# Performance work log

Measured on AMD Instinct MI355X. Metric: run time of the kernel, lower is better.

## Reference

```python
import jax, jax.numpy as jnp
import numpy as np

EPS = 1e-5

def _conv1x1(x, w, b):
    # x: (b,c,t,h,w), w: (o,c), b: (o,)  -> (b,o,t,h,w)
    return jnp.einsum('bcthw,oc->bothw', x, w) + b[None, :, None, None, None]

def setup_inputs() -> dict:
    key = jax.random.key(0)
    ks = jax.random.split(key, 12)
    B, C, IC, T, H, W = 32, 1024, 512, 8, 16, 8
    s_c = 1.0 / np.sqrt(C)
    s_ic = 1.0 / np.sqrt(IC)
    return {
        'x':       jax.random.normal(ks[0], (B, C, T, H, W), jnp.float32),
        'g_w':     jax.random.normal(ks[1], (IC, C), jnp.float32) * s_c,
        'g_b':     jax.random.normal(ks[2], (IC,), jnp.float32) * 0.01,
        'theta_w': jax.random.normal(ks[3], (IC, C), jnp.float32) * s_c,
        'theta_b': jax.random.normal(ks[4], (IC,), jnp.float32) * 0.01,
        'phi_w':   jax.random.normal(ks[5], (IC, C), jnp.float32) * s_c,
        'phi_b':   jax.random.normal(ks[6], (IC,), jnp.float32) * 0.01,
        'w_w':     jax.random.normal(ks[7], (C, IC), jnp.float32) * s_ic,
        'w_b':     jax.random.normal(ks[8], (C,), jnp.float32) * 0.01,
        'bn_gamma': jax.random.normal(ks[9], (C,), jnp.float32) * 0.1 + 1.0,
        'bn_beta':  jax.random.normal(ks[10], (C,), jnp.float32) * 0.01,
        'bn_mean':  jax.random.normal(ks[11], (C,), jnp.float32) * 0.01,
        'bn_var':   jnp.ones((C,), jnp.float32),
    }

def reference(x, g_w, g_b, theta_w, theta_b, phi_w, phi_b, w_w, w_b,
              bn_gamma, bn_beta, bn_mean, bn_var):
    B, C, T, H, W = x.shape
    IC = g_w.shape[0]
    # value projection, flattened per frame: (b, t, ic*h*w)
    g_x = _conv1x1(x, g_w, g_b)                       # (b,ic,t,h,w)
    g_x = jnp.transpose(g_x, (0, 2, 1, 3, 4)).reshape(B, T, IC * H * W)
    # pooled query/key over spatial dims: (b,t,ic) and (b,ic,t)
    theta = _conv1x1(x, theta_w, theta_b).mean(axis=(3, 4))   # (b,ic,t)
    phi = _conv1x1(x, phi_w, phi_b).mean(axis=(3, 4))         # (b,ic,t)
    f = jnp.einsum('bct,bcs->bts', theta, phi)                # (b,t,t)
    attn = jax.nn.softmax(f, axis=-1)
    y = jnp.einsum('bts,bsd->btd', attn, g_x)                 # (b,t,ic*h*w)
    y = jnp.transpose(y.reshape(B, T, IC, H, W), (0, 2, 1, 3, 4))  # (b,ic,t,h,w)
    # output projection + BatchNorm3d (inference stats) + residual
    wy = _conv1x1(y, w_w, w_b)                        # (b,c,t,h,w)
    inv = bn_gamma / jnp.sqrt(bn_var + EPS)
    wy = wy * inv[None, :, None, None, None] + (bn_beta - bn_mean * inv)[None, :, None, None, None]
    return wy + x
```

## Files before the change

### kernel.cpp

```cpp
#include <hip/hip_runtime.h>
#include <hip/hip_bf16.h>

typedef __attribute__((ext_vector_type(8))) short bf16x8;
typedef __attribute__((ext_vector_type(4))) float f32x4;

#if defined(__has_builtin)
#if __has_builtin(__builtin_amdgcn_global_load_lds)
#define USE_GLOAD_LDS 1
#endif
#endif

__device__ __forceinline__ void gload_lds16(const void* g, void* ldsbase) {
#ifdef USE_GLOAD_LDS
    __builtin_amdgcn_global_load_lds(
        (__attribute__((address_space(1))) void*)(g),
        (__attribute__((address_space(3))) void*)(ldsbase), 16, 0, 0);
#endif
}

__global__ __launch_bounds__(256) void early_kernel(
        const float* __restrict__ x, float* __restrict__ xbar,
        const float* __restrict__ gw, const float* __restrict__ ww,
        __hip_bfloat16* __restrict__ gwt, __hip_bfloat16* __restrict__ wwb,
        const float* __restrict__ gb, const float* __restrict__ wb,
        const float* __restrict__ gamma, const float* __restrict__ beta,
        const float* __restrict__ mean, const float* __restrict__ var,
        float* __restrict__ inv, float* __restrict__ shift) {
    __shared__ float tile[32][33];
    int bid = blockIdx.x;
    int tid = threadIdx.x;
    if (bid < 16384) {
        int row = bid * 16 + (tid >> 4);
        int j = tid & 15;
        const float4* p = (const float4*)(x + (size_t)row * 128);
        float4 a = p[j * 2], b2 = p[j * 2 + 1];
        float s = a.x + a.y + a.z + a.w + b2.x + b2.y + b2.z + b2.w;
        s += __shfl_xor(s, 1); s += __shfl_xor(s, 2);
        s += __shfl_xor(s, 4); s += __shfl_xor(s, 8);
        if (j == 0) xbar[row] = s * (1.0f / 128.0f);
    } else if (bid < 16896) {
        int b2 = bid - 16384;
        int icb = b2 >> 5, cb = b2 & 31;
        int r = tid >> 5, c = tid & 31;
        #pragma unroll
        for (int i = 0; i < 4; i++)
            tile[r + i * 8][c] = gw[(size_t)(icb * 32 + r + i * 8) * 1024 + cb * 32 + c];
        __syncthreads();
        #pragma unroll
        for (int i = 0; i < 4; i++) {
            int cin = cb * 32 + r + i * 8;
            gwt[(size_t)cin * 512 + icb * 32 + c] = __float2bfloat16(tile[c][r + i * 8]);
        }
    } else if (bid < 17152) {
        int b2 = bid - 16896;
        size_t base = (size_t)b2 * 2048 + (size_t)tid * 8;
        const float4* src = (const float4*)(ww + base);
        float4 v0 = src[0], v1 = src[1];
        __hip_bfloat16 tmp[8];
        tmp[0] = __float2bfloat16(v0.x); tmp[1] = __float2bfloat16(v0.y);
        tmp[2] = __float2bfloat16(v0.z); tmp[3] = __float2bfloat16(v0.w);
        tmp[4] = __float2bfloat16(v1.x); tmp[5] = __float2bfloat16(v1.y);
        tmp[6] = __float2bfloat16(v1.z); tmp[7] = __float2bfloat16(v1.w);
        *(bf16x8*)(wwb + base) = *(const bf16x8*)tmp;
    } else {
        int b2 = bid - 17152;
        int wv = tid >> 6, l = tid & 63;
        int c = b2 * 32 + wv * 8 + (l >> 3);
        int j = l & 7;
        const float* wr = ww + (size_t)c * 512;
        float acc = 0.0f;
        #pragma unroll 8
        for (int k = j; k < 512; k += 8) acc += wr[k] * gb[k];
        acc += __shfl_xor(acc, 1); acc += __shfl_xor(acc, 2); acc += __shfl_xor(acc, 4);
        if (j == 0) {
            float cb2 = wb[c] + acc;
            float iv = gamma[c] * rsqrtf(var[c] + 1e-5f);
            inv[c] = iv;
            shift[c] = cb2 * iv + beta[c] - mean[c] * iv;
        }
    }
}

__global__ __launch_bounds__(256) void stage2_kernel(
        const float* __restrict__ xbar,
        const float* __restrict__ tw, const float* __restrict__ tb,
        const float* __restrict__ pw, const float* __restrict__ pb,
        float* __restrict__ theta, float* __restrict__ phi,
        const __hip_bfloat16* __restrict__ wwb,
        const __hip_bfloat16* __restrict__ gwt,
        __hip_bfloat16* __restrict__ M) {
    __shared__ __align__(16) char smem[32768];
    int bid = blockIdx.x;
    int tid = threadIdx.x;
    if (bid < 1024) {
        float* xs = (float*)smem;
        int which = bid & 1;
        int icc = (bid >> 1) & 15;
        int b = bid >> 5;
        const float* w = which ? pw : tw;
        const float* bias = which ? pb : tb;
        float* out = which ? phi : theta;
        for (int i = tid; i < 8192; i += 256) xs[i] = xbar[b * 8192 + i];
        __syncthreads();
        int icl = tid >> 3;
        int t = tid & 7;
        int ic = icc * 32 + icl;
        const float* wr = w + (size_t)ic * 1024;
        float acc = 0.0f;
        #pragma unroll 8
        for (int k = 0; k < 1024; k++) acc += wr[k] * xs[k * 8 + t];
        out[((size_t)b * 512 + ic) * 8 + t] = acc + bias[ic];
    } else {
        __hip_bfloat16* As = (__hip_bfloat16*)smem;
        __hip_bfloat16* Bs = (__hip_bfloat16*)(smem + 8192);
        int b2 = bid - 1024;
        int mb = b2 >> 3, nb = b2 & 7;
        int c0 = mb * 128, n0 = nb * 128;
        int w = tid >> 6, l = tid & 63;
        int wr = w >> 1, wc = w & 1;
        const __hip_bfloat16* Ab = wwb + (size_t)c0 * 512;
        const __hip_bfloat16* Bb = gwt + (size_t)n0 * 512;
        int arow = tid >> 2, akq = tid & 3;
        f32x4 acc[4][4] = {};
        for (int kk = 0; kk < 16; ++kk) {
            int k0 = kk * 32;
#ifdef USE_GLOAD_LDS
            gload_lds16(Ab + (size_t)arow * 512 + k0 + akq * 8,        (char*)As + w * 1024);
            gload_lds16(Ab + (size_t)(arow + 64) * 512 + k0 + akq * 8, (char*)As + 4096 + w * 1024);
            gload_lds16(Bb + (size_t)arow * 512 + k0 + akq * 8,        (char*)Bs + w * 1024);
            gload_lds16(Bb + (size_t)(arow + 64) * 512 + k0 + akq * 8, (char*)Bs + 4096 + w * 1024);
#else
            *(bf16x8*)((char*)As + (size_t)tid * 16)        = *(const bf16x8*)(Ab + (size_t)arow * 512 + k0 + akq * 8);
            *(bf16x8*)((char*)As + 4096 + (size_t)tid * 16) = *(const bf16x8*)(Ab + (size_t)(arow + 64) * 512 + k0 + akq * 8);
            *(bf16x8*)((char*)Bs + (size_t)tid * 16)        = *(const bf16x8*)(Bb + (size_t)arow * 512 + k0 + akq * 8);
            *(bf16x8*)((char*)Bs + 4096 + (size_t)tid * 16) = *(const bf16x8*)(Bb + (size_t)(arow + 64) * 512 + k0 + akq * 8);
#endif
            __syncthreads();
            const __hip_bfloat16* Ap = As + ((size_t)(wr * 64 + (l & 15)) * 32) + (l >> 4) * 8;
            const __hip_bfloat16* Bp = Bs + ((size_t)(wc * 64 + (l & 15)) * 32) + (l >> 4) * 8;
            bf16x8 af[4], bfr[4];
            #pragma unroll
            for (int m = 0; m < 4; m++) af[m] = *(const bf16x8*)(Ap + m * 16 * 32);
            #pragma unroll
            for (int n = 0; n < 4; n++) bfr[n] = *(const bf16x8*)(Bp + n * 16 * 32);
            #pragma unroll
            for (int m = 0; m < 4; m++)
                #pragma unroll
                for (int n = 0; n < 4; n++)
                    acc[m][n] = __builtin_amdgcn_mfma_f32_16x16x32_bf16(af[m], bfr[n], acc[m][n], 0, 0, 0);
            __syncthreads();
        }
        int col = l & 15, rg = l >> 4;
        #pragma unroll
        for (int m = 0; m < 4; m++)
            #pragma unroll
            for (int j = 0; j < 4; j++) {
                int gc = c0 + wr * 64 + m * 16 + rg * 4 + j;
                #pragma unroll
                for (int n = 0; n < 4; n++)
                    M[(size_t)gc * 1024 + n0 + wc * 64 + n * 16 + col] = __float2bfloat16(acc[m][n][j]);
            }
    }
}

__global__ __launch_bounds__(64) void attn_kernel(const float* __restrict__ theta,
                                                  const float* __restrict__ phi,
                                                  float* __restrict__ attn) {
    __shared__ float th[4096], ph[4096];
    int b = blockIdx.x, lane = threadIdx.x;
    for (int i = lane; i < 4096; i += 64) {
        th[i] = theta[(size_t)b * 4096 + i];
        ph[i] = phi[(size_t)b * 4096 + i];
    }
    __syncthreads();
    int t = lane >> 3, s = lane & 7;
    float f = 0.0f;
    #pragma unroll 8
    for (int ic = 0; ic < 512; ic++) f += th[ic * 8 + t] * ph[ic * 8 + s];
    float m = f;
    m = fmaxf(m, __shfl_xor(m, 1));
    m = fmaxf(m, __shfl_xor(m, 2));
    m = fmaxf(m, __shfl_xor(m, 4));
    float e = __expf(f - m);
    float sum = e;
    sum += __shfl_xor(sum, 1); sum += __shfl_xor(sum, 2); sum += __shfl_xor(sum, 4);
    attn[b * 64 + lane] = e / sum;
}

__global__ __launch_bounds__(256) void mix_kernel(const float* __restrict__ x,
                                                  const float* __restrict__ attn,
                                                  __hip_bfloat16* __restrict__ xmt) {
    int orig = blockIdx.x;
    int wg = (orig & 7) * 64 + (orig >> 3);
    int b = wg >> 4;
    int hwg = wg & 15;
    __shared__ float at[64];
    __shared__ float xs[8][8][33];
    int tid = threadIdx.x;
    if (tid < 64) at[tid] = attn[b * 64 + tid];
    int ci = tid >> 3, s = tid & 7;
    int h = tid >> 5, cq = tid & 31;
    const float* xb = x + ((size_t)b << 20);
    __hip_bfloat16* ob = xmt + ((size_t)b << 20);
    for (int cc = 0; cc < 32; ++cc) {
        const float4* src = (const float4*)(xb + ((size_t)(cc * 32 + ci) * 8 + s) * 128 + hwg * 8);
        float4 v0 = src[0], v1 = src[1];
        __syncthreads();
        xs[s][0][ci] = v0.x; xs[s][1][ci] = v0.y; xs[s][2][ci] = v0.z; xs[s][3][ci] = v0.w;
        xs[s][4][ci] = v1.x; xs[s][5][ci] = v1.y; xs[s][6][ci] = v1.z; xs[s][7][ci] = v1.w;
        __syncthreads();
        float xr[8];
        #pragma unroll
        for (int ss = 0; ss < 8; ss++) xr[ss] = xs[ss][h][cq];
        #pragma unroll
        for (int t = 0; t < 8; t++) {
            float o = 0.0f;
            #pragma unroll
            for (int ss = 0; ss < 8; ss++) o += at[t * 8 + ss] * xr[ss];
            ob[(size_t)(t * 128 + hwg * 8 + h) * 1024 + cc * 32 + cq] = __float2bfloat16(o);
        }
    }
}

__global__ __launch_bounds__(256, 3) void gemm128_kernel(
        const __hip_bfloat16* __restrict__ Mw,
        const __hip_bfloat16* __restrict__ xmt,
        const float* __restrict__ x,
        const float* __restrict__ inv, const float* __restrict__ shift,
        float* __restrict__ out) {
    __shared__ __align__(16) __hip_bfloat16 HBs[16384];
    char* AH = (char*)HBs;
    const int BUFB = 16384;

    int orig = blockIdx.x;
    int bid = (orig & 7) * 256 + (orig >> 3);
    int b = bid >> 6;
    int mb = (bid >> 3) & 7;
    int nb = bid & 7;
    int c0 = mb * 128, n0 = nb * 128;

    int tid = threadIdx.x;
    int w = tid >> 6, l = tid & 63;
    int wr = w >> 1, wc = w & 1;

    int sgl = (((l & 3) - ((l >> 3) & 3)) & 3);
    const __hip_bfloat16* aS = Mw + (size_t)(c0 + w * 16 + (l >> 2)) * 1024 + sgl * 8;
    const __hip_bfloat16* bS = xmt + ((size_t)b << 20) + (size_t)(n0 + w * 16 + (l >> 2)) * 1024 + sgl * 8;
    int stBase = w * 1024;

    int rdSlot = ((l >> 4) + (((l & 15) >> 1) & 3)) & 3;
    int aRdBase = (wr * 64 + (l & 15)) * 64 + rdSlot * 16;
    int bRdBase = 8192 + (wc * 64 + (l & 15)) * 64 + rdSlot * 16;

    f32x4 acc[4][4] = {};

    #define ISSUE(q) do {                                                       \
        gload_lds16(aS,             AH + (q) * BUFB + stBase);                  \
        gload_lds16(aS + 64 * 1024, AH + (q) * BUFB + 4096 + stBase);           \
        gload_lds16(bS,             AH + (q) * BUFB + 8192 + stBase);           \
        gload_lds16(bS + 64 * 1024, AH + (q) * BUFB + 12288 + stBase);          \
        aS += 32; bS += 32;                                                     \
    } while (0)

    #define V4 asm volatile("s_waitcnt vmcnt(4)" ::: "memory")
    #define V0 asm volatile("s_waitcnt vmcnt(0)" ::: "memory")
    #define SB0 __builtin_amdgcn_sched_barrier(0)
    #define BAR __builtin_amdgcn_s_barrier()
    #define LGKM0 asm volatile("s_waitcnt lgkmcnt(0)" ::: "memory")

    #define HSTEP(q, MODE) do {                                                 \
        const char* bp = AH + (q) * BUFB;                                       \
        bf16x8 af0 = *(const bf16x8*)(bp + aRdBase);                            \
        bf16x8 af1 = *(const bf16x8*)(bp + aRdBase + 1024);                     \
        bf16x8 af2 = *(const bf16x8*)(bp + aRdBase + 2048);                     \
        bf16x8 af3 = *(const bf16x8*)(bp + aRdBase + 3072);                     \
        bf16x8 bf0 = *(const bf16x8*)(bp + bRdBase);                            \
        bf16x8 bf1 = *(const bf16x8*)(bp + bRdBase + 1024);                     \
        bf16x8 bf2 = *(const bf16x8*)(bp + bRdBase + 2048);                     \
        bf16x8 bf3 = *(const bf16x8*)(bp + bRdBase + 3072);                     \
        LGKM0; SB0;                                                             \
        BAR;                                  \
        if ((MODE) == 0) ISSUE(q);              \
        SB0;                                                                    \
        __builtin_amdgcn_s_setprio(1);                                          \
        _Pragma("unroll")                                                       \
        for (int n = 0; n < 4; ++n) {                                           \
            bf16x8 bfn = (n == 0) ? bf0 : (n == 1) ? bf1 : (n == 2) ? bf2 : bf3;\
            acc[0][n] = __builtin_amdgcn_mfma_f32_16x16x32_bf16(af0, bfn, acc[0][n], 0, 0, 0); \
            acc[1][n] = __builtin_amdgcn_mfma_f32_16x16x32_bf16(af1, bfn, acc[1][n], 0, 0, 0); \
            acc[2][n] = __builtin_amdgcn_mfma_f32_16x16x32_bf16(af2, bfn, acc[2][n], 0, 0, 0); \
            acc[3][n] = __builtin_amdgcn_mfma_f32_16x16x32_bf16(af3, bfn, acc[3][n], 0, 0, 0); \
        }                                                                       \
        __builtin_amdgcn_s_setprio(0);                                          \
        SB0;                                                                    \
        if ((MODE) == 0) { V4; BAR; SB0; }                                      \
        else if ((MODE) == 1) { V0; BAR; SB0; }                                 \
    } while (0)

    ISSUE(0); ISSUE(1);
    V4; BAR; SB0;

    #pragma unroll 1
    for (int t = 0; t < 15; ++t) {
        HSTEP(0, 0);
        HSTEP(1, 0);
    }
    HSTEP(0, 1);
    HSTEP(1, 2);

    #undef ISSUE
    #undef HSTEP
    #undef V4
    #undef V0
    #undef SB0
    #undef BAR
    #undef LGKM0

    int col = l & 15, rg = l >> 4;
    const float* xb = x + ((size_t)b << 20);
    float* ob = out + ((size_t)b << 20);
    #pragma unroll
    for (int mi = 0; mi < 4; ++mi) {
        #pragma unroll
        for (int j = 0; j < 4; ++j) {
            int gc = c0 + wr * 64 + mi * 16 + rg * 4 + j;
            float iv = inv[gc], sh = shift[gc];
            size_t rowoff = (size_t)gc * 1024 + n0 + wc * 64 + col;
            #pragma unroll
            for (int n = 0; n < 4; ++n) {
                size_t idx = rowoff + n * 16;
                ob[idx] = acc[mi][n][j] * iv + sh + xb[idx];
            }
        }
    }
}

extern "C" void kernel_launch(void* const* d_in, const int* in_sizes, int n_in,
                              void* d_out, int out_size, void* d_ws, size_t ws_size,
                              hipStream_t stream) {
    const float* x    = (const float*)d_in[0];
    const float* g_w  = (const float*)d_in[1];
    const float* g_b  = (const float*)d_in[2];
    const float* th_w = (const float*)d_in[3];
    const float* th_b = (const float*)d_in[4];
    const float* ph_w = (const float*)d_in[5];
    const float* ph_b = (const float*)d_in[6];
    const float* w_w  = (const float*)d_in[7];
    const float* w_b  = (const float*)d_in[8];
    const float* gam  = (const float*)d_in[9];
    const float* bet  = (const float*)d_in[10];
    const float* mea  = (const float*)d_in[11];
    const float* var  = (const float*)d_in[12];
    float* out = (float*)d_out;
    char* ws = (char*)d_ws;

    __hip_bfloat16* xmt = (__hip_bfloat16*)ws;
    __hip_bfloat16* Mw  = (__hip_bfloat16*)(ws + 67108864);
    float* xbar  = (float*)(ws + 69206016);
    float* theta = (float*)(ws + 70254592);
    float* phi   = (float*)(ws + 70778880);
    float* attn  = (float*)(ws + 71303168);
    float* inv   = (float*)(ws + 71311360);
    float* shift = (float*)(ws + 71315456);
    __hip_bfloat16* gwt = (__hip_bfloat16*)ws;
    __hip_bfloat16* wwb = (__hip_bfloat16*)(ws + 1048576);

    hipLaunchKernelGGL(early_kernel, dim3(17184), dim3(256), 0, stream,
                       x, xbar, g_w, w_w, gwt, wwb,
                       g_b, w_b, gam, bet, mea, var, inv, shift);
    hipLaunchKernelGGL(stage2_kernel, dim3(1088), dim3(256), 0, stream,
                       xbar, th_w, th_b, ph_w, ph_b, theta, phi, wwb, gwt, Mw);
    hipLaunchKernelGGL(attn_kernel, dim3(32), dim3(64), 0, stream, theta, phi, attn);
    hipLaunchKernelGGL(mix_kernel, dim3(512), dim3(256), 0, stream, x, attn, xmt);
    hipLaunchKernelGGL(gemm128_kernel, dim3(2048), dim3(256), 0, stream,
                       Mw, xmt, x, inv, shift, out);
}
```

Baseline: 233.5 us.

## Restructure mix kernel tiling and vectorize theta/phi projection loads

The mix kernel now assigns each block a 32-channel slab of one batch. It loads the whole slab contiguously with float4 reads, converts it to bf16 in LDS, and applies the temporal attention mixing for all spatial positions, using twice as many blocks. The theta/phi projection in stage2 transposes xbar into a padded t-major LDS layout so that both weights and activations can be read as float4 with two accumulators. The aim is coalesced global reads and fewer barriers, at the cost of more LDS per block in mix, which may limit occupancy. Rounding x to bf16 before mixing, rather than after, slightly changes numerics.

Measured after the change: 219.6 us. 1.06x faster.

```diff
diff --git a/kernel.cpp b/kernel.cpp
--- a/kernel.cpp
+++ b/kernel.cpp
@@ -16,6 +16,11 @@
         (__attribute__((address_space(1))) void*)(g),
         (__attribute__((address_space(3))) void*)(ldsbase), 16, 0, 0);
 #endif
+}
+
+__device__ __forceinline__ unsigned short f2bf(float f) {
+    __hip_bfloat16 h = __float2bfloat16(f);
+    return *reinterpret_cast<unsigned short*>(&h);
 }
 
 __global__ __launch_bounds__(256) void early_kernel(
@@ -89,7 +94,7 @@
         const __hip_bfloat16* __restrict__ wwb,
         const __hip_bfloat16* __restrict__ gwt,
         __hip_bfloat16* __restrict__ M) {
-    __shared__ __align__(16) char smem[32768];
+    __shared__ __align__(16) char smem[33024];
     int bid = blockIdx.x;
     int tid = threadIdx.x;
     if (bid < 1024) {
@@ -100,16 +105,36 @@
         const float* w = which ? pw : tw;
         const float* bias = which ? pb : tb;
         float* out = which ? phi : theta;
-        for (int i = tid; i < 8192; i += 256) xs[i] = xbar[b * 8192 + i];
+        const float* xbb = xbar + b * 8192;
+        #pragma unroll
+        for (int k = 0; k < 8; ++k) {
+            int f4 = tid + k * 256;
+            float4 v = *(const float4*)(xbb + (size_t)f4 * 4);
+            int c = f4 >> 1;
+            int t0 = (f4 & 1) * 4;
+            xs[(t0 + 0) * 1028 + c] = v.x;
+            xs[(t0 + 1) * 1028 + c] = v.y;
+            xs[(t0 + 2) * 1028 + c] = v.z;
+            xs[(t0 + 3) * 1028 + c] = v.w;
+        }
         __syncthreads();
-        int icl = tid >> 3;
-        int t = tid & 7;
+        int icl = tid >> 3, t = tid & 7;
         int ic = icc * 32 + icl;
         const float* wr = w + (size_t)ic * 1024;
-        float acc = 0.0f;
-        #pragma unroll 8
-        for (int k = 0; k < 1024; k++) acc += wr[k] * xs[k * 8 + t];
-        out[((size_t)b * 512 + ic) * 8 + t] = acc + bias[ic];
+        const float* xr = xs + t * 1028;
+        float a0 = 0.0f, a1 = 0.0f;
+        #pragma unroll 4
+        for (int k = 0; k < 1024; k += 8) {
+            float4 wv0 = *(const float4*)(wr + k);
+            float4 wv1 = *(const float4*)(wr + k + 4);
+            float4 xv0 = *(const float4*)(xr + k);
+            float4 xv1 = *(const float4*)(xr + k + 4);
+            a0 = fmaf(wv0.x, xv0.x, a0); a0 = fmaf(wv0.y, xv0.y, a0);
+            a0 = fmaf(wv0.z, xv0.z, a0); a0 = fmaf(wv0.w, xv0.w, a0);
+            a1 = fmaf(wv1.x, xv1.x, a1); a1 = fmaf(wv1.y, xv1.y, a1);
+            a1 = fmaf(wv1.z, xv1.z, a1); a1 = fmaf(wv1.w, xv1.w, a1);
+        }
+        out[((size_t)b * 512 + ic) * 8 + t] = a0 + a1 + bias[ic];
     } else {
         __hip_bfloat16* As = (__hip_bfloat16*)smem;
         __hip_bfloat16* Bs = (__hip_bfloat16*)(smem + 8192);
@@ -191,33 +216,49 @@
                                                   const float* __restrict__ attn,
                                                   __hip_bfloat16* __restrict__ xmt) {
     int orig = blockIdx.x;
-    int wg = (orig & 7) * 64 + (orig >> 3);
-    int b = wg >> 4;
-    int hwg = wg & 15;
+    int wg = (orig & 7) * 128 + (orig >> 3);
+    int b = wg >> 5;
+    int c0 = (wg & 31) * 32;
     __shared__ float at[64];
-    __shared__ float xs[8][8][33];
+    __shared__ __align__(8) unsigned short xls[32 * 1028];
     int tid = threadIdx.x;
     if (tid < 64) at[tid] = attn[b * 64 + tid];
-    int ci = tid >> 3, s = tid & 7;
-    int h = tid >> 5, cq = tid & 31;
-    const float* xb = x + ((size_t)b << 20);
-    __hip_bfloat16* ob = xmt + ((size_t)b << 20);
-    for (int cc = 0; cc < 32; ++cc) {
-        const float4* src = (const float4*)(xb + ((size_t)(cc * 32 + ci) * 8 + s) * 128 + hwg * 8);
-        float4 v0 = src[0], v1 = src[1];
-        __syncthreads();
-        xs[s][0][ci] = v0.x; xs[s][1][ci] = v0.y; xs[s][2][ci] = v0.z; xs[s][3][ci] = v0.w;
-        xs[s][4][ci] = v1.x; xs[s][5][ci] = v1.y; xs[s][6][ci] = v1.z; xs[s][7][ci] = v1.w;
-        __syncthreads();
-        float xr[8];
-        #pragma unroll
-        for (int ss = 0; ss < 8; ss++) xr[ss] = xs[ss][h][cq];
-        #pragma unroll
-        for (int t = 0; t < 8; t++) {
-            float o = 0.0f;
-            #pragma unroll
-            for (int ss = 0; ss < 8; ss++) o += at[t * 8 + ss] * xr[ss];
-            ob[(size_t)(t * 128 + hwg * 8 + h) * 1024 + cc * 32 + cq] = __float2bfloat16(o);
+    const float* xb = x + ((size_t)b << 20) + (size_t)c0 * 1024;
+    #pragma unroll
+    for (int k = 0; k < 32; ++k) {
+        int f4 = tid + k * 256;
+        float4 v = *(const float4*)(xb + (size_t)f4 * 4);
+        int ci = f4 >> 8;
+        int rem = (f4 & 255) * 4;
+        unsigned short h[4];
+        h[0] = f2bf(v.x); h[1] = f2bf(v.y); h[2] = f2bf(v.z); h[3] = f2bf(v.w);
+        *(ushort4*)(&xls[ci * 1028 + rem]) = *(const ushort4*)h;
+    }
+    __syncthreads();
+    int ci = tid & 31, h2 = tid >> 5;
+    const unsigned short* basep = &xls[ci * 1028];
+    __hip_bfloat16* ob = xmt + ((size_t)b << 20) + c0 + ci;
+    #pragma unroll
+    for (int i = 0; i < 8; ++i) {
+        int hw0 = (h2 + 8 * i) * 2;
+        float o0[8] = {}, o1[8] = {};
+        #pragma unroll
+        for (int s = 0; s < 8; ++s) {
+            unsigned int pr = *(const unsigned int*)(basep + s * 128 + hw0);
+            float v0 = __uint_as_float(pr << 16);
+            float v1 = __uint_as_float(pr & 0xffff0000u);
+            #pragma unroll
+            for (int t = 0; t < 8; ++t) {
+                float a = at[t * 8 + s];
+                o0[t] = fmaf(a, v0, o0[t]);
+                o1[t] = fmaf(a, v1, o1[t]);
+            }
+        }
+        #pragma unroll
+        for (int t = 0; t < 8; ++t) {
+            size_t nn = (size_t)(t * 128 + hw0) * 1024;
+            ob[nn] = __float2bfloat16(o0[t]);
+            ob[nn + 1024] = __float2bfloat16(o1[t]);
         }
     }
 }
@@ -279,8 +320,8 @@
         bf16x8 bf2 = *(const bf16x8*)(bp + bRdBase + 2048);                     \
         bf16x8 bf3 = *(const bf16x8*)(bp + bRdBase + 3072);                     \
         LGKM0; SB0;                                                             \
-        BAR;                                  \
-        if ((MODE) == 0) ISSUE(q);              \
+        BAR;                                                                    \
+        if ((MODE) == 0) ISSUE(q);                                              \
         SB0;                                                                    \
         __builtin_amdgcn_s_setprio(1);                                          \
         _Pragma("unroll")                                                       \
@@ -371,7 +412,7 @@
     hipLaunchKernelGGL(stage2_kernel, dim3(1088), dim3(256), 0, stream,
                        xbar, th_w, th_b, ph_w, ph_b, theta, phi, wwb, gwt, Mw);
     hipLaunchKernelGGL(attn_kernel, dim3(32), dim3(64), 0, stream, theta, phi, attn);
-    hipLaunchKernelGGL(mix_kernel, dim3(512), dim3(256), 0, stream, x, attn, xmt);
+    hipLaunchKernelGGL(mix_kernel, dim3(1024), dim3(256), 0, stream, x, attn, xmt);
     hipLaunchKernelGGL(gemm128_kernel, dim3(2048), dim3(256), 0, stream,
                        Mw, xmt, x, inv, shift, out);
 }
```
